# Kernel optimization log

Hardware: AMD Instinct MI355X
Metric: run time of the kernel (lower is better)

The kernel has to match this reference:

```python
import jax, jax.numpy as jnp
import numpy as np

FS = 44100
RESAMPLING_FACTOR = 32
N_SINES = 256
TWO_PI = 2.0 * np.pi


def linear_upsample(x, scale):
    """Match torch F.interpolate(mode='linear', align_corners=False) with integer scale_factor.
    x: [B, C, N] -> [B, C, N*scale]
    """
    n = x.shape[-1]
    out_n = n * scale
    # source coordinate for each output index (area-pixel convention)
    src = (jnp.arange(out_n, dtype=jnp.float32) + 0.5) / scale - 0.5
    src = jnp.clip(src, 0.0, n - 1)
    i0 = jnp.floor(src).astype(jnp.int32)
    i1 = jnp.minimum(i0 + 1, n - 1)
    w = (src - i0.astype(jnp.float32)).astype(x.dtype)
    return x[..., i0] * (1.0 - w) + x[..., i1] * w


def setup_inputs() -> dict:
    key = jax.random.key(0)
    k1, k2 = jax.random.split(key)
    B, S, N = 4, N_SINES, 512
    # realistic audible frequencies and normalized amplitudes
    frequencies = jax.random.uniform(k1, (B, S, N), dtype=jnp.float32) * 5000.0 + 40.0
    amplitudes = jax.random.uniform(k2, (B, S, N), dtype=jnp.float32) / S
    return {"frequencies": frequencies, "amplitudes": amplitudes}


def reference(frequencies, amplitudes):
    # upsample control signals: [B, S, N] -> [B, S, N*R]
    freqs_up = linear_upsample(frequencies, RESAMPLING_FACTOR)
    amps_up = linear_upsample(amplitudes, RESAMPLING_FACTOR)
    omegas = freqs_up * (TWO_PI / FS)
    phases = jnp.cumsum(omegas, axis=-1)
    phases = phases % TWO_PI
    # weighted sum over sines, keepdim -> [B, 1, N*R]
    signal = jnp.sum(amps_up * jnp.sin(phases), axis=1, keepdims=True)
    return signal
```

## Files before the change

### kernel.cpp

```cpp
#include <hip/hip_runtime.h>
#include <hip/hip_bf16.h>

constexpr int S = 256;
constexpr int N = 512;
constexpr int R = 32;
constexpr int OUT_N = N * R;

__global__ __launch_bounds__(512) void block_prefix_kernel(
    const float* __restrict__ freq, double* __restrict__ G) {
  const int row = blockIdx.x;
  const int n = threadIdx.x;
  const float* f = freq + (size_t)row * N;

  __shared__ double sh[N];
  float fn  = f[n];
  float fnp = (n < N - 1) ? f[n + 1] : 0.0f;
  sh[n] = (n < N - 1) ? 16.0 * ((double)fn + (double)fnp) : 0.0;
  __syncthreads();

  for (int off = 1; off < N; off <<= 1) {
    double add = (n >= off) ? sh[n - off] : 0.0;
    __syncthreads();
    sh[n] += add;
    __syncthreads();
  }

  double g = 16.0 * (double)f[0] + ((n == 0) ? 0.0 : sh[n - 1]);
  G[(size_t)row * N + n] = g;
}

__global__ __launch_bounds__(256) void synth_kernel(
    const float* __restrict__ freq, const float* __restrict__ amp,
    const double* __restrict__ G, float* __restrict__ out) {
  const int tid = threadIdx.x;
  const int split = tid >> 6;
  const int samp = tid & 63;
  const int gid = blockIdx.x * 64 + samp;
  const int b = gid >> 14;
  const int j = gid & (OUT_N - 1);

  int n;
  double c1, c2, gsel;
  float wa;
  if (j < 16) {
    n = 0; c1 = (double)(j + 1); c2 = 0.0; gsel = 0.0; wa = 0.0f;
  } else if (j >= OUT_N - 16) {
    n = N - 1; c1 = (double)(j - (OUT_N - 16) + 1); c2 = 0.0; gsel = 1.0; wa = 0.0f;
  } else {
    const int jj = j - 16;
    n = jj >> 5;
    const int k = jj & 31;
    c1 = (double)(k + 1);
    c2 = (double)((k + 1) * (k + 1)) * (1.0 / 64.0);
    gsel = 1.0;
    wa = ((float)k + 0.5f) * (1.0f / 32.0f);
  }
  const int dn1 = min(n + 1, N - 1) - n;

  const float* frow = freq + ((size_t)b * S) * N + n;
  const float* arow = amp  + ((size_t)b * S) * N + n;
  const double* grow = G   + ((size_t)b * S) * N + n;

  const double inv_fs = 1.0 / 44100.0;
  float acc = 0.0f;
  const int s0 = split * (S / 4);
  #pragma unroll 4
  for (int s = s0; s < s0 + S / 4; ++s) {
    const float* fp = frow + (size_t)s * N;
    const float* ap = arow + (size_t)s * N;
    const float fn  = fp[0];
    const float fn1 = fp[dn1];
    const float an  = ap[0];
    const float an1 = ap[dn1];
    const double g = grow[(size_t)s * N];

    double ph = fma(gsel, g, fma(c1, (double)fn,
                                 c2 * ((double)fn1 - (double)fn)));
    double r = ph * inv_fs;
    r -= floor(r);
    const float sv = __builtin_amdgcn_sinf((float)r);
    const float av = fmaf(an1 - an, wa, an);
    acc = fmaf(av, sv, acc);
  }

  __shared__ float red[256];
  red[tid] = acc;
  __syncthreads();
  if (tid < 64) {
    const float v = red[tid] + red[tid + 64] + red[tid + 128] + red[tid + 192];
    out[gid] = v;
  }
}

extern "C" void kernel_launch(void* const* d_in, const int* in_sizes, int n_in,
                              void* d_out, int out_size, void* d_ws, size_t ws_size,
                              hipStream_t stream) {
  const float* freq = (const float*)d_in[0];
  const float* amp  = (const float*)d_in[1];
  float* out = (float*)d_out;
  double* G = (double*)d_ws;

  const int B = in_sizes[0] / (S * N);

  block_prefix_kernel<<<dim3(B * S), dim3(512), 0, stream>>>(freq, G);
  synth_kernel<<<dim3(B * OUT_N / 64), dim3(256), 0, stream>>>(freq, amp, G, out);
}
```

Measured before the change: 77.56 us.

## Precompute per-sample phase fraction and packed coefficients in s-major layout, use fp32 synth

The prefix kernel now reduces the cumulative phase to a fractional cycle in double and writes packed float4 (phase frac, f, df, a) plus da in a [b][n][s] layout. The synth loop then reads contiguous vectors along the sine axis and does only fp32 math, instead of five strided loads and FP64 fma/floor per sine. This removes expensive double-precision work and uncoalesced gathers from the hot loop. The cost is a larger workspace write in the prep pass and slightly lower precision in the per-sample phase offset.

```diff
diff --git a/kernel.cpp b/kernel.cpp
--- a/kernel.cpp
+++ b/kernel.cpp
@@ -6,16 +6,23 @@
 constexpr int R = 32;
 constexpr int OUT_N = N * R;
 
-__global__ __launch_bounds__(512) void block_prefix_kernel(
-    const float* __restrict__ freq, double* __restrict__ G) {
+__global__ __launch_bounds__(512) void prep_kernel(
+    const float* __restrict__ freq, const float* __restrict__ amp,
+    float4* __restrict__ P4, float* __restrict__ P1) {
   const int row = blockIdx.x;
   const int n = threadIdx.x;
+  const int b = row / S;
+  const int s = row - b * S;
   const float* f = freq + (size_t)row * N;
+  const float* a = amp  + (size_t)row * N;
+
+  const float fn  = f[n];
+  const float fn1 = (n < N - 1) ? f[n + 1] : fn;
+  const float an  = a[n];
+  const float an1 = (n < N - 1) ? a[n + 1] : an;
 
   __shared__ double sh[N];
-  float fn  = f[n];
-  float fnp = (n < N - 1) ? f[n + 1] : 0.0f;
-  sh[n] = (n < N - 1) ? 16.0 * ((double)fn + (double)fnp) : 0.0;
+  sh[n] = (n < N - 1) ? 16.0 * ((double)fn + (double)fn1) : 0.0;
   __syncthreads();
 
   for (int off = 1; off < N; off <<= 1) {
@@ -25,13 +32,19 @@
     __syncthreads();
   }
 
-  double g = 16.0 * (double)f[0] + ((n == 0) ? 0.0 : sh[n - 1]);
-  G[(size_t)row * N + n] = g;
+  const double G = 16.0 * (double)f[0] + ((n == 0) ? 0.0 : sh[n - 1]);
+  double q = G * (1.0 / 44100.0);
+  q -= floor(q);
+  const float gfrac = (float)q;
+
+  const size_t o = ((size_t)(b * N + n)) * S + s;
+  P4[o] = make_float4(gfrac, fn, fn1 - fn, an);
+  P1[o] = an1 - an;
 }
 
 __global__ __launch_bounds__(256) void synth_kernel(
-    const float* __restrict__ freq, const float* __restrict__ amp,
-    const double* __restrict__ G, float* __restrict__ out) {
+    const float4* __restrict__ P4, const float* __restrict__ P1,
+    float* __restrict__ out) {
   const int tid = threadIdx.x;
   const int split = tid >> 6;
   const int samp = tid & 63;
@@ -40,46 +53,38 @@
   const int j = gid & (OUT_N - 1);
 
   int n;
-  double c1, c2, gsel;
-  float wa;
+  float c1, c2, gsel, wa;
   if (j < 16) {
-    n = 0; c1 = (double)(j + 1); c2 = 0.0; gsel = 0.0; wa = 0.0f;
+    n = 0; c1 = (float)(j + 1); c2 = 0.0f; gsel = 0.0f; wa = 0.0f;
   } else if (j >= OUT_N - 16) {
-    n = N - 1; c1 = (double)(j - (OUT_N - 16) + 1); c2 = 0.0; gsel = 1.0; wa = 0.0f;
+    n = N - 1; c1 = (float)(j - (OUT_N - 16) + 1); c2 = 0.0f; gsel = 1.0f; wa = 0.0f;
   } else {
     const int jj = j - 16;
     n = jj >> 5;
     const int k = jj & 31;
-    c1 = (double)(k + 1);
-    c2 = (double)((k + 1) * (k + 1)) * (1.0 / 64.0);
-    gsel = 1.0;
+    c1 = (float)(k + 1);
+    c2 = (float)((k + 1) * (k + 1)) * (1.0f / 64.0f);
+    gsel = 1.0f;
     wa = ((float)k + 0.5f) * (1.0f / 32.0f);
   }
-  const int dn1 = min(n + 1, N - 1) - n;
+  const float inv_fs = 1.0f / 44100.0f;
+  c1 *= inv_fs;
+  c2 *= inv_fs;
 
-  const float* frow = freq + ((size_t)b * S) * N + n;
-  const float* arow = amp  + ((size_t)b * S) * N + n;
-  const double* grow = G   + ((size_t)b * S) * N + n;
+  const size_t base = ((size_t)(b * N + n)) * S;
+  const float4* __restrict__ p4 = P4 + base;
+  const float*  __restrict__ p1 = P1 + base;
 
-  const double inv_fs = 1.0 / 44100.0;
   float acc = 0.0f;
   const int s0 = split * (S / 4);
-  #pragma unroll 4
+  #pragma unroll 8
   for (int s = s0; s < s0 + S / 4; ++s) {
-    const float* fp = frow + (size_t)s * N;
-    const float* ap = arow + (size_t)s * N;
-    const float fn  = fp[0];
-    const float fn1 = fp[dn1];
-    const float an  = ap[0];
-    const float an1 = ap[dn1];
-    const double g = grow[(size_t)s * N];
-
-    double ph = fma(gsel, g, fma(c1, (double)fn,
-                                 c2 * ((double)fn1 - (double)fn)));
-    double r = ph * inv_fs;
-    r -= floor(r);
-    const float sv = __builtin_amdgcn_sinf((float)r);
-    const float av = fmaf(an1 - an, wa, an);
+    const float4 v = p4[s];
+    const float da = p1[s];
+    float r = fmaf(c2, v.z, fmaf(c1, v.y, v.x * gsel));
+    r -= floorf(r);
+    const float sv = __builtin_amdgcn_sinf(r);
+    const float av = fmaf(da, wa, v.w);
     acc = fmaf(av, sv, acc);
   }
 
@@ -87,8 +92,7 @@
   red[tid] = acc;
   __syncthreads();
   if (tid < 64) {
-    const float v = red[tid] + red[tid + 64] + red[tid + 128] + red[tid + 192];
-    out[gid] = v;
+    out[gid] = red[tid] + red[tid + 64] + red[tid + 128] + red[tid + 192];
   }
 }
 
@@ -98,10 +102,11 @@
   const float* freq = (const float*)d_in[0];
   const float* amp  = (const float*)d_in[1];
   float* out = (float*)d_out;
-  double* G = (double*)d_ws;
 
   const int B = in_sizes[0] / (S * N);
+  float4* P4 = (float4*)d_ws;
+  float*  P1 = (float*)((char*)d_ws + (size_t)B * N * S * sizeof(float4));
 
-  block_prefix_kernel<<<dim3(B * S), dim3(512), 0, stream>>>(freq, G);
-  synth_kernel<<<dim3(B * OUT_N / 64), dim3(256), 0, stream>>>(freq, amp, G, out);
+  prep_kernel<<<dim3(B * S), dim3(512), 0, stream>>>(freq, amp, P4, P1);
+  synth_kernel<<<dim3(B * OUT_N / 64), dim3(256), 0, stream>>>(P4, P1, out);
 }
```

After: 80.18 us. 1.03x slower.
